# Optimization experiments

Hardware: AMD Instinct MI355X
Metric: run time of the kernel (lower is better)

The kernel has to match this reference:

```python
import jax, jax.numpy as jnp
import numpy as np

V, E, H, D = 10000, 256, 512, 768  # vocab, embed, hidden(=attn), encoder dims
B, T, N = 32, 128, 196


def setup_inputs() -> dict:
    key = jax.random.key(0)
    ks = jax.random.split(key, 16)
    s = 0.02
    inp = {
        "x": jax.random.randint(ks[0], (B, T), 0, V),
        "enc_mem": jax.random.normal(ks[1], (B, N, D), dtype=jnp.float32),
        "enc_mask": jnp.ones((B, N), dtype=jnp.int32),
        # parameters, stored (in, out) so y = x @ W
        "emb_table": jax.random.normal(ks[2], (V, E), dtype=jnp.float32) * s,
        "We": jax.random.normal(ks[3], (D, H), dtype=jnp.float32) * s,   # attn.W_e
        "Wh": jax.random.normal(ks[4], (H, H), dtype=jnp.float32) * s,   # attn.W_h
        "v": jax.random.normal(ks[5], (H,), dtype=jnp.float32) * s,      # attn.v
        "Wih": jax.random.normal(ks[6], (E + D, 4 * H), dtype=jnp.float32) * s,
        "Whh": jax.random.normal(ks[7], (H, 4 * H), dtype=jnp.float32) * s,
        "bih": jnp.zeros((4 * H,), dtype=jnp.float32),
        "bhh": jnp.zeros((4 * H,), dtype=jnp.float32),
        "fcW": jax.random.normal(ks[8], (H, V), dtype=jnp.float32) * s,
        "fcb": jnp.zeros((V,), dtype=jnp.float32),
        "W2h": jax.random.normal(ks[9], (D, H), dtype=jnp.float32) * s,  # enc_to_h
        "b2h": jnp.zeros((H,), dtype=jnp.float32),
        "W2c": jax.random.normal(ks[10], (D, H), dtype=jnp.float32) * s,  # enc_to_c
        "b2c": jnp.zeros((H,), dtype=jnp.float32),
    }
    return inp


def _decode(x, enc_mem, enc_mask, emb_table, We, Wh, v, Wih, Whh, bih, bhh,
            fcW, fcb, W2h, b2h, W2c, b2c):
    emb = emb_table[x]                       # (B,T,E); dropout=0 (eval)
    pooled = enc_mem.mean(axis=1)            # (B,D)
    h = jnp.tanh(pooled @ W2h + b2h)         # init_hidden
    c = jnp.tanh(pooled @ W2c + b2c)
    Ke = jnp.einsum('bnd,dh->bnh', enc_mem, We)  # precompute W_e(enc_mem)
    neg = jnp.float32(-1e9)
    mask0 = (enc_mask == 0)

    def step(carry, e_t):
        h, c = carry
        energy = jnp.tanh((h @ Wh)[:, None, :] + Ke)        # (B,N,H)
        scores = jnp.einsum('bnh,h->bn', energy, v)         # (B,N)
        scores = jnp.where(mask0, neg, scores)
        alpha = jax.nn.softmax(scores, axis=-1)
        context = jnp.einsum('bn,bnd->bd', alpha, enc_mem)  # (B,D)
        lstm_in = jnp.concatenate([e_t, context], axis=-1)  # (B,E+D)
        gates = lstm_in @ Wih + bih + h @ Whh + bhh         # (B,4H)
        i_g, f_g, g_g, o_g = jnp.split(gates, 4, axis=-1)   # torch order i,f,g,o
        c_new = jax.nn.sigmoid(f_g) * c + jax.nn.sigmoid(i_g) * jnp.tanh(g_g)
        h_new = jax.nn.sigmoid(o_g) * jnp.tanh(c_new)
        logit = h_new @ fcW + fcb                           # (B,V)
        return (h_new, c_new), logit

    (h, c), logits_t = jax.lax.scan(step, (h, c), jnp.swapaxes(emb, 0, 1))
    logits = jnp.swapaxes(logits_t, 0, 1)                   # (B,T,V)
    return logits, h, c


def reference(x, enc_mem, enc_mask, emb_table, We, Wh, v, Wih, Whh, bih, bhh,
              fcW, fcb, W2h, b2h, W2c, b2c):
    return _decode(x, enc_mem, enc_mask, emb_table, We, Wh, v, Wih, Whh,
                   bih, bhh, fcW, fcb, W2h, b2h, W2c, b2c)
```

## Files before the change

kernel.cpp:

```cpp
#include <hip/hip_runtime.h>

typedef unsigned short u16;
typedef __attribute__((ext_vector_type(8))) short short8;
typedef __attribute__((ext_vector_type(4))) float f32x4;
typedef __attribute__((ext_vector_type(4))) unsigned int u32x4;

#define B_  32
#define T_  128
#define N_  196
#define D_  768
#define E_  256
#define H_  512
#define V_  10000
#define G4H 2048
#define NBLK 256
#define BH  (B_ * H_)
#define BD  (B_ * D_)

#define O_ENCBF 0UL
#define O_WHT   9633792UL
#define O_WHHT  10158080UL
#define O_WIHDT 12255232UL
#define O_KE    15400960UL
#define O_GEMB  21823488UL
#define O_BSUM  38600704UL
#define O_CT    38608896UL
#define O_HIST  38674432UL
#define O_HX2   42868736UL
#define O_HWX   42934272UL
#define O_CTXA  42999808UL
#define O_DEN   43196416UL
#define O_BARS  43196672UL
#define O_REL   43198720UL

__device__ __forceinline__ float b2f(u16 u) {
  union { unsigned i; float f; } c; c.i = ((unsigned)u) << 16; return c.f;
}
__device__ __forceinline__ u16 f2b(float f) {
  unsigned u = __float_as_uint(f);
  unsigned r = (u + 0x7fffu + ((u >> 16) & 1u)) >> 16;
  return (u16)r;
}
__device__ __forceinline__ float fast_tanh(float x) {
  float e = __expf(2.f * x);
  return 1.f - 2.f * __builtin_amdgcn_rcpf(e + 1.f);
}
__device__ __forceinline__ float sigm(float x) {
  return __builtin_amdgcn_rcpf(1.f + __expf(-x));
}
__device__ __forceinline__ float wred_sum(float x) {
  #pragma unroll
  for (int o = 32; o; o >>= 1) x += __shfl_xor(x, o, 64);
  return x;
}

__device__ __forceinline__ float ld_bypass_f32(const float* p) {
  float v;
  asm volatile("global_load_dword %0, %1, off sc0 sc1\n\ts_waitcnt vmcnt(0)"
               : "=v"(v) : "v"(p) : "memory");
  return v;
}
__device__ __forceinline__ unsigned ld_bypass_u32(const unsigned* p) {
  unsigned v;
  asm volatile("global_load_dword %0, %1, off sc0 sc1\n\ts_waitcnt vmcnt(0)"
               : "=v"(v) : "v"(p) : "memory");
  return v;
}
__device__ __forceinline__ void ld2_bypass(const void* p0, const void* p1,
                                           u32x4& a, u32x4& b) {
  asm volatile(
    "global_load_dwordx4 %0, %2, off sc0 sc1\n\t"
    "global_load_dwordx4 %1, %3, off sc0 sc1\n\t"
    "s_waitcnt vmcnt(0)"
    : "=&v"(a), "=&v"(b) : "v"(p0), "v"(p1) : "memory");
}
__device__ __forceinline__ void ld6_1_bypass(
    const void* p0, const void* p1, const void* p2, const void* p3,
    const void* p4, const void* p5, const void* pd,
    u32x4& a, u32x4& b, u32x4& c, u32x4& d, u32x4& e, u32x4& f, float& dv) {
  asm volatile(
    "global_load_dwordx4 %0, %7, off sc0 sc1\n\t"
    "global_load_dwordx4 %1, %8, off sc0 sc1\n\t"
    "global_load_dwordx4 %2, %9, off sc0 sc1\n\t"
    "global_load_dwordx4 %3, %10, off sc0 sc1\n\t"
    "global_load_dwordx4 %4, %11, off sc0 sc1\n\t"
    "global_load_dwordx4 %5, %12, off sc0 sc1\n\t"
    "global_load_dword %6, %13, off sc0 sc1\n\t"
    "s_waitcnt vmcnt(0)"
    : "=&v"(a), "=&v"(b), "=&v"(c), "=&v"(d), "=&v"(e), "=&v"(f), "=&v"(dv)
    : "v"(p0), "v"(p1), "v"(p2), "v"(p3), "v"(p4), "v"(p5), "v"(pd)
    : "memory");
}
__device__ __forceinline__ void st_bypass_f32(float* p, float v) {
  asm volatile("global_store_dword %0, %1, off sc0 sc1" :: "v"(p), "v"(v) : "memory");
}
__device__ __forceinline__ void st_bypass_u32(unsigned* p, unsigned v) {
  asm volatile("global_store_dword %0, %1, off sc0 sc1" :: "v"(p), "v"(v) : "memory");
}
__device__ __forceinline__ void st_bypass_u16(u16* p, u16 v) {
  unsigned vv = v;
  asm volatile("global_store_short %0, %1, off sc0 sc1" :: "v"(p), "v"(vv) : "memory");
}

__device__ __forceinline__ unsigned bar_sum16(const unsigned* p) {
  unsigned a0,a1,a2,a3,a4,a5,a6,a7,a8,a9,a10,a11,a12,a13,a14,a15;
  asm volatile(
    "global_load_dword %0, %16, off sc0 sc1\n\t"
    "global_load_dword %1, %16, off offset:128 sc0 sc1\n\t"
    "global_load_dword %2, %16, off offset:256 sc0 sc1\n\t"
    "global_load_dword %3, %16, off offset:384 sc0 sc1\n\t"
    "global_load_dword %4, %16, off offset:512 sc0 sc1\n\t"
    "global_load_dword %5, %16, off offset:640 sc0 sc1\n\t"
    "global_load_dword %6, %16, off offset:768 sc0 sc1\n\t"
    "global_load_dword %7, %16, off offset:896 sc0 sc1\n\t"
    "global_load_dword %8, %16, off offset:1024 sc0 sc1\n\t"
    "global_load_dword %9, %16, off offset:1152 sc0 sc1\n\t"
    "global_load_dword %10, %16, off offset:1280 sc0 sc1\n\t"
    "global_load_dword %11, %16, off offset:1408 sc0 sc1\n\t"
    "global_load_dword %12, %16, off offset:1536 sc0 sc1\n\t"
    "global_load_dword %13, %16, off offset:1664 sc0 sc1\n\t"
    "global_load_dword %14, %16, off offset:1792 sc0 sc1\n\t"
    "global_load_dword %15, %16, off offset:1920 sc0 sc1\n\t"
    "s_waitcnt vmcnt(0)"
    : "=&v"(a0), "=&v"(a1), "=&v"(a2), "=&v"(a3), "=&v"(a4), "=&v"(a5),
      "=&v"(a6), "=&v"(a7), "=&v"(a8), "=&v"(a9), "=&v"(a10), "=&v"(a11),
      "=&v"(a12), "=&v"(a13), "=&v"(a14), "=&v"(a15)
    : "v"(p) : "memory");
  return ((a0+a1)+(a2+a3)) + ((a4+a5)+(a6+a7)) +
         ((a8+a9)+(a10+a11)) + ((a12+a13)+(a14+a15));
}

__device__ __forceinline__ void gridbar(unsigned* bars, unsigned* rel,
                                        int bid, unsigned target) {
  __syncthreads();
  if (bid == 0) {
    if (threadIdx.x == 0) {
      asm volatile("s_waitcnt vmcnt(0) lgkmcnt(0)" ::: "memory");
      __hip_atomic_fetch_add(bars, 1u, __ATOMIC_RELAXED, __HIP_MEMORY_SCOPE_AGENT);
      while (bar_sum16(bars) < target) __builtin_amdgcn_s_sleep(1);
    }
    __syncthreads();
    if (threadIdx.x < NBLK) st_bypass_u32(rel + (size_t)threadIdx.x * 32, target);
  } else {
    if (threadIdx.x == 0) {
      asm volatile("s_waitcnt vmcnt(0) lgkmcnt(0)" ::: "memory");
      __hip_atomic_fetch_add(bars + (size_t)(bid & 15) * 32, 1u,
                             __ATOMIC_RELAXED, __HIP_MEMORY_SCOPE_AGENT);
      while (ld_bypass_u32(rel + (size_t)bid * 32) < target)
        __builtin_amdgcn_s_sleep(2);
    }
    __syncthreads();
  }
}


__global__ void conv_bf(const float* __restrict__ in, u16* __restrict__ out, int n) {
  int i = blockIdx.x * blockDim.x + threadIdx.x;
  int st = gridDim.x * blockDim.x;
  for (; i < n; i += st) out[i] = f2b(in[i]);
}

__global__ void bsum_k(const float* __restrict__ a, const float* __restrict__ b,
                       float* __restrict__ o, int n) {
  int i = blockIdx.x * blockDim.x + threadIdx.x;
  if (i < n) o[i] = a[i] + b[i];
}

__global__ void transpose_bf(const float* __restrict__ in, u16* __restrict__ out, int R, int C) {
  __shared__ float tl[64][65];
  int tid = threadIdx.x;
  int tc0 = blockIdx.x * 64, tr0 = blockIdx.y * 64;
  int cc = tid & 63;
  for (int rr = tid >> 6; rr < 64; rr += 4) {
    int rg = tr0 + rr, cg = tc0 + cc;
    tl[rr][cc] = (rg < R && cg < C) ? in[(size_t)rg * C + cg] : 0.f;
  }
  __syncthreads();
  int rr = tid & 63;
  for (int c2 = tid >> 6; c2 < 64; c2 += 4) {
    int cg = tc0 + c2, rg = tr0 + rr;
    if (cg < C && rg < R) out[(size_t)cg * R + rg] = f2b(tl[rr][c2]);
  }
}

__global__ __launch_bounds__(512) void init_hc(
    const float* __restrict__ enc, const float* __restrict__ W2h,
    const float* __restrict__ b2h, const float* __restrict__ W2c,
    const float* __restrict__ b2c, u16* __restrict__ hx2, float* __restrict__ cT)
{
  __shared__ float pool[D_];
  int b = blockIdx.x, tid = threadIdx.x;
  for (int d = tid; d < D_; d += 512) {
    float s = 0.f;
    const float* ep = enc + (size_t)b * N_ * D_ + d;
    for (int n = 0; n < N_; ++n) s += ep[(size_t)n * D_];
    pool[d] = s * (1.f / 196.f);
  }
  __syncthreads();
  float a = b2h[tid], a2 = b2c[tid];
  #pragma unroll 4
  for (int d = 0; d < D_; ++d) {
    float pv = pool[d];
    a  += pv * W2h[d * H_ + tid];
    a2 += pv * W2c[d * H_ + tid];
  }
  hx2[b * H_ + tid] = f2b(fast_tanh(a));
  cT[b * H_ + tid] = fast_tanh(a2);
}

template<int AMODE, int OUTMODE, int BIAS>
__global__ __launch_bounds__(256) void gemm2(
    const void* __restrict__ Av, const float* __restrict__ Bf,
    const int* __restrict__ xidx, void* __restrict__ Cv,
    const float* __restrict__ bias, int M, int N, int K, int lda)
{
  __shared__ __align__(16) u16 Al[128][72];
  __shared__ __align__(16) u16 Bl[128][72];
  const int tid = threadIdx.x;
  const int tm0 = blockIdx.y * 128, tn0 = blockIdx.x * 128;
  const int wv = tid >> 6, lane = tid & 63;
  const int wr = wv >> 1, wc = wv & 1;
  f32x4 acc[4][4] = {};
  const int r = tid >> 1, cb = (tid & 1) * 32;
  const int bkr = tid >> 5;
  const int bnc = (tid & 31) * 4;
  for (int k0 = 0; k0 < K; k0 += 64) {
    int rm = tm0 + r; if (rm >= M) rm = M - 1;
    if (AMODE == 0) {
      const u16* gp = (const u16*)Av + (size_t)rm * lda + k0 + cb;
      #pragma unroll
      for (int u = 0; u < 4; ++u)
        *(short8*)&Al[r][cb + u * 8] = *(const short8*)(gp + u * 8);
    } else {
      const float* gp = (const float*)Av + (size_t)xidx[rm] * lda + k0 + cb;
      #pragma unroll
      for (int u = 0; u < 4; ++u) {
        f32x4 a0 = *(const f32x4*)(gp + u * 8);
        f32x4 a1 = *(const f32x4*)(gp + u * 8 + 4);
        Al[r][cb + u * 8 + 0] = f2b(a0[0]); Al[r][cb + u * 8 + 1] = f2b(a0[1]);
        Al[r][cb + u * 8 + 2] = f2b(a0[2]); Al[r][cb + u * 8 + 3] = f2b(a0[3]);
        Al[r][cb + u * 8 + 4] = f2b(a1[0]); Al[r][cb + u * 8 + 5] = f2b(a1[1]);
        Al[r][cb + u * 8 + 6] = f2b(a1[2]); Al[r][cb + u * 8 + 7] = f2b(a1[3]);
      }
    }
    {
      int ncc = tn0 + bnc; if (ncc > N - 4) ncc = N - 4;
      #pragma unroll
      for (int u = 0; u < 8; ++u) {
        int kr = bkr + u * 8;
        const float* bp = Bf + (size_t)(k0 + kr) * N + ncc;
        f32x4 bv = *(const f32x4*)bp;
        #pragma unroll
        for (int j = 0; j < 4; ++j) Bl[bnc + j][kr] = f2b(bv[j]);
      }
    }
    __syncthreads();
    #pragma unroll
    for (int kk = 0; kk < 64; kk += 32) {
      short8 af[4], bfv[4];
      #pragma unroll
      for (int i = 0; i < 4; ++i)
        af[i] = *(const short8*)&Al[wr * 64 + i * 16 + (lane & 15)][kk + (lane >> 4) * 8];
      #pragma unroll
      for (int j = 0; j < 4; ++j)
        bfv[j] = *(const short8*)&Bl[wc * 64 + j * 16 + (lane & 15)][kk + (lane >> 4) * 8];
      #pragma unroll
      for (int i = 0; i < 4; ++i)
        #pragma unroll
        for (int j = 0; j < 4; ++j)
          acc[i][j] = __builtin_amdgcn_mfma_f32_16x16x32_bf16(af[i], bfv[j], acc[i][j], 0, 0, 0);
    }
    __syncthreads();
  }
  #pragma unroll
  for (int i = 0; i < 4; ++i) {
    int row0 = tm0 + wr * 64 + i * 16 + (lane >> 4) * 4;
    #pragma unroll
    for (int j = 0; j < 4; ++j) {
      int col = tn0 + wc * 64 + j * 16 + (lane & 15);
      if (col < N) {
        float bs = BIAS ? bias[col] : 0.f;
        #pragma unroll
        for (int rr2 = 0; rr2 < 4; ++rr2) {
          int row = row0 + rr2;
          if (row < M) {
            float val = acc[i][j][rr2] + bs;
            if (OUTMODE == 0) ((float*)Cv)[(size_t)row * N + col] = val;
            else if (OUTMODE == 1) ((u16*)Cv)[(size_t)row * N + col] = f2b(val);
            else {
              int tt = row & 127, bb = row >> 7;
              ((u16*)Cv)[((size_t)tt * G4H + col) * 32 + bb] = f2b(val);
            }
          }
        }
      }
    }
  }
}

__global__ __launch_bounds__(512, 1) void recur9(
    const u16* __restrict__ enc_bf, const int* __restrict__ mask,
    const u16* __restrict__ Ke, const u16* __restrict__ WhT,
    const float* __restrict__ vvec, const u16* __restrict__ WhhT,
    const u16* __restrict__ WihDT, const u16* __restrict__ g_emb,
    const float* __restrict__ cT0,
    u16* hx2, float* hwx, float* ctxAcc, float* denom,
    u16* h_hist, float* out_h, float* out_c, unsigned* bars, unsigned* rel)
{
  __shared__ u32x4 hst16[64 * 16];
  __shared__ union {
    struct { float part1[8][64]; } p1;
    struct { float hw8[512]; float e[32]; } p2;
    struct { u32x4 ctx16[96 * 16]; f32x4 part3[8][69]; } p3;
  } su;
  __shared__ float gpre[16][16];
  __shared__ float cfl[4][16];
  __shared__ float maskf[32];

  const int bid = blockIdx.x, tid = threadIdx.x;
  const int lane = tid & 63, wvx = tid >> 6;
  const int b = bid >> 3, s8 = bid & 7;
  const int n0 = s8 * 25;
  const int nmax = min(25, N_ - n0);
  const int bh = bid >> 7, hb4 = bid & 127;
  const int b_base = bh * 16, hx4 = hb4 * 4;
  const int n16 = lane & 15, kh = lane >> 4;
  const int gcol = (n16 >> 2) * H_ + hx4 + (n16 & 3);
  const int hb16 = tid & 15, hc4 = (tid >> 4) & 3, hks = tid >> 6;
  const int hwc = hb4 * 4 + hc4;
  const int bl = tid & 15, kc0 = tid >> 4;
  const int ro = tid & 15, co = tid >> 4;

  float vreg[8];
  #pragma unroll
  for (int j = 0; j < 8; ++j) vreg[j] = vvec[lane * 8 + j];
  if (tid < nmax) maskf[tid] = (mask[b * N_ + n0 + tid] == 0) ? 0.f : 1.f;
  if (tid < 64) cfl[tid >> 4][tid & 15] =
      cT0[(b_base + (tid & 15)) * H_ + hx4 + (tid >> 4)];

  short8 wf[5];
  #pragma unroll
  for (int i = 0; i < 5; ++i) {
    int ks = wvx * 5 + i;
    if (ks < 16) wf[i] = *(const short8*)(WhhT + (size_t)gcol * H_ + ks * 32 + kh * 8);
    else         wf[i] = *(const short8*)(WihDT + (size_t)gcol * D_ + (ks - 16) * 32 + kh * 8);
  }
  short8 wh8[8];
  #pragma unroll
  for (int i = 0; i < 8; ++i)
    wh8[i] = *(const short8*)(WhT + (size_t)hwc * H_ + hks * 64 + i * 8);
  short8 kvp[4];
  #pragma unroll
  for (int i = 0; i < 4; ++i) {
    int nn = wvx + i * 8; if (nn >= nmax) nn = nmax - 1;
    kvp[i] = *(const short8*)(Ke + ((size_t)(b * N_ + n0 + nn)) * H_ + lane * 8);
  }
  __syncthreads();

  unsigned tgt = 0;
  for (int t = 0; t < T_; ++t) {
    const int rb = t & 1, wb = rb ^ 1;
    const int cbuf = t & 1, nbuf = cbuf ^ 1;
    {
      const u16* hp = hx2 + (size_t)rb * BH + (b_base + bl) * H_;
      u32x4 v0, v1;
      ld2_bypass(hp + kc0 * 8, hp + (kc0 + 32) * 8, v0, v1);
      hst16[(kc0     ) * 16 + bl] = v0;
      hst16[(kc0 + 32) * 16 + bl] = v1;
    }
    __syncthreads();
    {
      float acc = 0.f;
      #pragma unroll
      for (int i = 0; i < 8; ++i) {
        short8 hb8 = *(const short8*)&hst16[(hks * 8 + i) * 16 + hb16];
        #pragma unroll
        for (int j = 0; j < 8; ++j)
          acc += b2f((u16)wh8[i][j]) * b2f((u16)hb8[j]);
      }
      su.p1.part1[hks][hc4 * 16 + hb16] = acc;
    }
    __syncthreads();
    if (tid < 64) {
      float s = 0.f;
      #pragma unroll
      for (int w = 0; w < 8; ++w) s += su.p1.part1[w][tid];
      st_bypass_f32(hwx + (size_t)(b_base + (tid & 15)) * H_ + hb4 * 4 + (tid >> 4), s);
    }
    tgt += NBLK;
    f32x4 gacc = {0.f, 0.f, 0.f, 0.f};
    float ge_pf = 0.f;
    __syncthreads();
    if (tid == 0) {
      asm volatile("s_waitcnt vmcnt(0) lgkmcnt(0)" ::: "memory");
      __hip_atomic_fetch_add(bars + (size_t)(bid & 15) * 32, 1u,
                             __ATOMIC_RELAXED, __HIP_MEMORY_SCOPE_AGENT);
    }
    if (bid == 0) {
      if (tid == 0) { while (bar_sum16(bars) < tgt) __builtin_amdgcn_s_sleep(1); }
      __syncthreads();
      if (tid < NBLK) st_bypass_u32(rel + (size_t)tid * 32, tgt);
      #pragma unroll
      for (int i = 0; i < 5; ++i) {
        int ks = wvx * 5 + i;
        if (ks < 16)
          gacc = __builtin_amdgcn_mfma_f32_16x16x32_bf16(
              *(const short8*)&hst16[(ks * 4 + kh) * 16 + n16], wf[i], gacc, 0, 0, 0);
      }
      if (tid < 256) {
        int gco = (co >> 2) * H_ + hx4 + (co & 3);
        ge_pf = b2f(g_emb[((size_t)t * G4H + gco) * 32 + (b_base + ro)]);
      }
    } else {
      #pragma unroll
      for (int i = 0; i < 5; ++i) {
        int ks = wvx * 5 + i;
        if (ks < 16)
          gacc = __builtin_amdgcn_mfma_f32_16x16x32_bf16(
              *(const short8*)&hst16[(ks * 4 + kh) * 16 + n16], wf[i], gacc, 0, 0, 0);
      }
      if (tid < 256) {
        int gco = (co >> 2) * H_ + hx4 + (co & 3);
        ge_pf = b2f(g_emb[((size_t)t * G4H + gco) * 32 + (b_base + ro)]);
      }
      __syncthreads();
      if (tid == 0) {
        while (ld_bypass_u32(rel + (size_t)bid * 32) < tgt)
          __builtin_amdgcn_s_sleep(2);
      }
      __syncthreads();
    }

    su.p2.hw8[(tid & 7) * 64 + (tid >> 3)] = ld_bypass_f32(hwx + b * H_ + tid);
    if (tid >= 25 && tid < 32) su.p2.e[tid] = 0.f;
    __syncthreads();
    #pragma unroll
    for (int i = 0; i < 4; ++i) {
      int nn = wvx + i * 8;
      if (nn < nmax) {
        float p = 0.f;
        #pragma unroll
        for (int j = 0; j < 8; ++j)
          p += vreg[j] * fast_tanh(su.p2.hw8[j * 64 + lane] + b2f((u16)kvp[i][j]));
        p = wred_sum(p);
        if (lane == 0) su.p2.e[nn] = maskf[nn] * __expf(p);
      }
    }
    __syncthreads();
    if (wvx == 0) {
      float sp = (lane < 25) ? su.p2.e[lane] : 0.f;
      sp = wred_sum(sp);
      if (lane == 0) atomicAdd(denom + cbuf * 32 + b, sp);
    }
    if (tid < 384) {
      float a0 = 0.f, a1 = 0.f;
      const u16* ep0 = enc_bf + ((size_t)(b * N_ + n0)) * D_ + 2 * tid;
      #pragma unroll
      for (int nn = 0; nn < 25; ++nn) {
        int nn_c = (nn < nmax) ? nn : 0;
        float ev = su.p2.e[nn];
        unsigned w = *(const unsigned*)(ep0 + (size_t)nn_c * D_);
        a0 += ev * b2f((u16)(w & 0xffffu));
        a1 += ev * b2f((u16)(w >> 16));
      }
      float* cp = ctxAcc + (size_t)cbuf * BD + b * D_ + 2 * tid;
      atomicAdd(cp, a0);
      atomicAdd(cp + 1, a1);
    }
    tgt += NBLK; gridbar(bars, rel, bid, tgt);

    {
      const float* cp = ctxAcc + (size_t)cbuf * BD + (size_t)(b_base + bl) * D_;
      u32x4 ca[3][2]; float dv;
      ld6_1_bypass(cp + (kc0     ) * 8, cp + (kc0     ) * 8 + 4,
                   cp + (kc0 + 32) * 8, cp + (kc0 + 32) * 8 + 4,
                   cp + (kc0 + 64) * 8, cp + (kc0 + 64) * 8 + 4,
                   denom + cbuf * 32 + (b_base + bl),
                   ca[0][0], ca[0][1], ca[1][0], ca[1][1],
                   ca[2][0], ca[2][1], dv);
      float rdv = 1.f / dv;
      #pragma unroll
      for (int r2 = 0; r2 < 3; ++r2) {
        int kc = kc0 + r2 * 32;
        u32x4 pk;
        #pragma unroll
        for (int hh = 0; hh < 2; ++hh) {
          float x0 = __uint_as_float(ca[r2][hh][0]) * rdv;
          float x1 = __uint_as_float(ca[r2][hh][1]) * rdv;
          float x2 = __uint_as_float(ca[r2][hh][2]) * rdv;
          float x3 = __uint_as_float(ca[r2][hh][3]) * rdv;
          pk[hh * 2]     = (unsigned)f2b(x0) | ((unsigned)f2b(x1) << 16);
          pk[hh * 2 + 1] = (unsigned)f2b(x2) | ((unsigned)f2b(x3) << 16);
        }
        su.p3.ctx16[kc * 16 + bl] = pk;
      }
    }
    __syncthreads();
    #pragma unroll
    for (int i = 0; i < 5; ++i) {
      int ks = wvx * 5 + i;
      if (ks >= 16)
        gacc = __builtin_amdgcn_mfma_f32_16x16x32_bf16(
            *(const short8*)&su.p3.ctx16[((ks - 16) * 4 + kh) * 16 + n16], wf[i],
            gacc, 0, 0, 0);
    }
    *(f32x4*)&su.p3.part3[wvx][lane] = gacc;
    __syncthreads();
    if (tid < 256) {
      int lp = ((ro >> 2) << 4) | co;
      float v = su.p3.part3[0][lp][ro & 3] + su.p3.part3[1][lp][ro & 3]
              + su.p3.part3[2][lp][ro & 3] + su.p3.part3[3][lp][ro & 3]
              + su.p3.part3[4][lp][ro & 3] + su.p3.part3[5][lp][ro & 3]
              + su.p3.part3[6][lp][ro & 3] + su.p3.part3[7][lp][ro & 3];
      gpre[co][ro] = v + ge_pf;
    }
    __syncthreads();
    if (tid < 64) {
      int row = tid & 15, j = tid >> 4;
      float gI = gpre[j][row], gF = gpre[4 + j][row];
      float gG = gpre[8 + j][row], gO = gpre[12 + j][row];
      float co2 = cfl[j][row];
      float cn = sigm(gF) * co2 + sigm(gI) * fast_tanh(gG);
      float hn = sigm(gO) * fast_tanh(cn);
      cfl[j][row] = cn;
      int bgl = b_base + row, hidx = hx4 + j;
      st_bypass_u16(hx2 + (size_t)wb * BH + bgl * H_ + hidx, f2b(hn));
      h_hist[((size_t)(bgl * T_ + t)) * H_ + hidx] = f2b(hn);
      if (t == T_ - 1) {
        out_h[bgl * H_ + hidx] = hn;
        out_c[bgl * H_ + hidx] = cn;
      }
    }
    tgt += NBLK;
    __syncthreads();
    if (tid == 0) {
      asm volatile("s_waitcnt vmcnt(0) lgkmcnt(0)" ::: "memory");
      __hip_atomic_fetch_add(bars + (size_t)(bid & 15) * 32, 1u,
                             __ATOMIC_RELAXED, __HIP_MEMORY_SCOPE_AGENT);
    }
    if (bid == 0) {
      if (tid == 0) { while (bar_sum16(bars) < tgt) __builtin_amdgcn_s_sleep(1); }
      __syncthreads();
      if (tid < NBLK) st_bypass_u32(rel + (size_t)tid * 32, tgt);
      if (tid < 96) st_bypass_f32(ctxAcc + (size_t)nbuf * BD + bid * 96 + tid, 0.f);
      if (tid < 32) st_bypass_f32(denom + nbuf * 32 + tid, 0.f);
    } else {
      if (tid < 96) st_bypass_f32(ctxAcc + (size_t)nbuf * BD + bid * 96 + tid, 0.f);
      __syncthreads();
      if (tid == 0) {
        while (ld_bypass_u32(rel + (size_t)bid * 32) < tgt)
          __builtin_amdgcn_s_sleep(2);
      }
      __syncthreads();
    }
  }
}

extern "C" void kernel_launch(void* const* d_in, const int* in_sizes, int n_in,
                              void* d_out, int out_size, void* d_ws, size_t ws_size,
                              hipStream_t stream) {
  const int*   x    = (const int*)d_in[0];
  const float* enc  = (const float*)d_in[1];
  const int*   mask = (const int*)d_in[2];
  const float* emb  = (const float*)d_in[3];
  const float* We   = (const float*)d_in[4];
  const float* Wh   = (const float*)d_in[5];
  const float* v    = (const float*)d_in[6];
  const float* Wih  = (const float*)d_in[7];
  const float* Whh  = (const float*)d_in[8];
  const float* bih  = (const float*)d_in[9];
  const float* bhh  = (const float*)d_in[10];
  const float* fcW  = (const float*)d_in[11];
  const float* fcb  = (const float*)d_in[12];
  const float* W2h  = (const float*)d_in[13];
  const float* b2h  = (const float*)d_in[14];
  const float* W2c  = (const float*)d_in[15];
  const float* b2c  = (const float*)d_in[16];
  float* out = (float*)d_out;

  char* ws = (char*)d_ws;
  u16* enc_bf = (u16*)(ws + O_ENCBF);
  u16* WhT    = (u16*)(ws + O_WHT);
  u16* WhhT   = (u16*)(ws + O_WHHT);
  u16* WihDT  = (u16*)(ws + O_WIHDT);
  u16* Ke     = (u16*)(ws + O_KE);
  u16* g_emb  = (u16*)(ws + O_GEMB);
  float* bsum = (float*)(ws + O_BSUM);
  float* cT   = (float*)(ws + O_CT);
  u16* h_hist = (u16*)(ws + O_HIST);
  u16* hx2    = (u16*)(ws + O_HX2);
  float* hwx  = (float*)(ws + O_HWX);
  float* ctxAcc = (float*)(ws + O_CTXA);
  float* denom  = (float*)(ws + O_DEN);
  unsigned* bars = (unsigned*)(ws + O_BARS);
  unsigned* rel  = (unsigned*)(ws + O_REL);
  float* out_h = out + (size_t)B_ * T_ * V_;
  float* out_c = out_h + B_ * H_;

  hipMemsetAsync(bars, 0, 2048, stream);
  hipMemsetAsync(rel, 0, 32768, stream);
  hipMemsetAsync(ctxAcc, 0, 196608, stream);
  hipMemsetAsync(denom, 0, 256, stream);
  conv_bf<<<1024, 256, 0, stream>>>(enc, enc_bf, B_ * N_ * D_);
  transpose_bf<<<dim3(8, 8), 256, 0, stream>>>(Wh, WhT, H_, H_);
  transpose_bf<<<dim3(32, 8), 256, 0, stream>>>(Whh, WhhT, H_, G4H);
  transpose_bf<<<dim3(32, 12), 256, 0, stream>>>(Wih + (size_t)E_ * G4H, WihDT, D_, G4H);
  bsum_k<<<8, 256, 0, stream>>>(bih, bhh, bsum, G4H);
  init_hc<<<32, 512, 0, stream>>>(enc, W2h, b2h, W2c, b2c, hx2, cT);
  gemm2<0, 1, 0><<<dim3(4, 49), 256, 0, stream>>>(enc_bf, We, nullptr, (void*)Ke,
                                                  nullptr, B_ * N_, H_, D_, D_);
  gemm2<1, 3, 1><<<dim3(16, 32), 256, 0, stream>>>(emb, Wih, x, (void*)g_emb,
                                                   bsum, B_ * T_, G4H, E_, E_);
  recur9<<<NBLK, 512, 0, stream>>>(enc_bf, mask, Ke, WhT, v, WhhT, WihDT, g_emb,
                                   cT, hx2, hwx, ctxAcc, denom,
                                   h_hist, out_h, out_c, bars, rel);
  gemm2<0, 0, 1><<<dim3(79, 32), 256, 0, stream>>>(h_hist, fcW, nullptr, (void*)out,
                                                   fcb, B_ * T_, V_, H_, H_);
}
```

Before: 2.512 ms.

## Replace master-polled grid barrier with hierarchical last-arriver release

The grid barrier no longer has block 0 repeatedly summing 16 counters before releasing everyone. Each block atomically increments its group counter, and the last arriver in a group bumps a summary counter. Whichever block arrives last overall writes the release flags for all 256 blocks. This removes the master's polling latency from the critical path of each of the three barriers per timestep, at the cost of serial release stores from a single thread and an extra atomic on the summary counter.

Result: slower. 3.357 ms (+33.6%).

```diff
diff --git a/kernel.cpp b/kernel.cpp
--- a/kernel.cpp
+++ b/kernel.cpp
@@ -32,6 +32,7 @@
 #define O_DEN   43196416UL
 #define O_BARS  43196672UL
 #define O_REL   43198720UL
+#define O_SUM   43231488UL
 
 __device__ __forceinline__ float b2f(u16 u) {
   union { unsigned i; float f; } c; c.i = ((unsigned)u) << 16; return c.f;
@@ -102,55 +103,30 @@
   asm volatile("global_store_short %0, %1, off sc0 sc1" :: "v"(p), "v"(vv) : "memory");
 }
 
-__device__ __forceinline__ unsigned bar_sum16(const unsigned* p) {
-  unsigned a0,a1,a2,a3,a4,a5,a6,a7,a8,a9,a10,a11,a12,a13,a14,a15;
-  asm volatile(
-    "global_load_dword %0, %16, off sc0 sc1\n\t"
-    "global_load_dword %1, %16, off offset:128 sc0 sc1\n\t"
-    "global_load_dword %2, %16, off offset:256 sc0 sc1\n\t"
-    "global_load_dword %3, %16, off offset:384 sc0 sc1\n\t"
-    "global_load_dword %4, %16, off offset:512 sc0 sc1\n\t"
-    "global_load_dword %5, %16, off offset:640 sc0 sc1\n\t"
-    "global_load_dword %6, %16, off offset:768 sc0 sc1\n\t"
-    "global_load_dword %7, %16, off offset:896 sc0 sc1\n\t"
-    "global_load_dword %8, %16, off offset:1024 sc0 sc1\n\t"
-    "global_load_dword %9, %16, off offset:1152 sc0 sc1\n\t"
-    "global_load_dword %10, %16, off offset:1280 sc0 sc1\n\t"
-    "global_load_dword %11, %16, off offset:1408 sc0 sc1\n\t"
-    "global_load_dword %12, %16, off offset:1536 sc0 sc1\n\t"
-    "global_load_dword %13, %16, off offset:1664 sc0 sc1\n\t"
-    "global_load_dword %14, %16, off offset:1792 sc0 sc1\n\t"
-    "global_load_dword %15, %16, off offset:1920 sc0 sc1\n\t"
-    "s_waitcnt vmcnt(0)"
-    : "=&v"(a0), "=&v"(a1), "=&v"(a2), "=&v"(a3), "=&v"(a4), "=&v"(a5),
-      "=&v"(a6), "=&v"(a7), "=&v"(a8), "=&v"(a9), "=&v"(a10), "=&v"(a11),
-      "=&v"(a12), "=&v"(a13), "=&v"(a14), "=&v"(a15)
-    : "v"(p) : "memory");
-  return ((a0+a1)+(a2+a3)) + ((a4+a5)+(a6+a7)) +
-         ((a8+a9)+(a10+a11)) + ((a12+a13)+(a14+a15));
-}
-
-__device__ __forceinline__ void gridbar(unsigned* bars, unsigned* rel,
-                                        int bid, unsigned target) {
+__device__ __forceinline__ void bar_arrive(unsigned* bars, unsigned* summary,
+                                           unsigned* rel, int bid, unsigned bk) {
   __syncthreads();
-  if (bid == 0) {
-    if (threadIdx.x == 0) {
-      asm volatile("s_waitcnt vmcnt(0) lgkmcnt(0)" ::: "memory");
-      __hip_atomic_fetch_add(bars, 1u, __ATOMIC_RELAXED, __HIP_MEMORY_SCOPE_AGENT);
-      while (bar_sum16(bars) < target) __builtin_amdgcn_s_sleep(1);
-    }
-    __syncthreads();
-    if (threadIdx.x < NBLK) st_bypass_u32(rel + (size_t)threadIdx.x * 32, target);
-  } else {
-    if (threadIdx.x == 0) {
-      asm volatile("s_waitcnt vmcnt(0) lgkmcnt(0)" ::: "memory");
-      __hip_atomic_fetch_add(bars + (size_t)(bid & 15) * 32, 1u,
-                             __ATOMIC_RELAXED, __HIP_MEMORY_SCOPE_AGENT);
-      while (ld_bypass_u32(rel + (size_t)bid * 32) < target)
-        __builtin_amdgcn_s_sleep(2);
-    }
-    __syncthreads();
-  }
+  if (threadIdx.x == 0) {
+    asm volatile("s_waitcnt vmcnt(0) lgkmcnt(0)" ::: "memory");
+    unsigned r = __hip_atomic_fetch_add(bars + (size_t)(bid & 15) * 32, 1u,
+                                        __ATOMIC_RELAXED, __HIP_MEMORY_SCOPE_AGENT);
+    if (r + 1u == 16u * bk) {
+      unsigned s = __hip_atomic_fetch_add(summary, 1u, __ATOMIC_RELAXED,
+                                          __HIP_MEMORY_SCOPE_AGENT);
+      if (s + 1u == 16u * bk) {
+        #pragma unroll 8
+        for (int i = 0; i < NBLK; ++i)
+          st_bypass_u32(rel + (size_t)i * 32, bk);
+      }
+    }
+  }
+}
+__device__ __forceinline__ void bar_wait(unsigned* rel, int bid, unsigned bk) {
+  if (threadIdx.x == 0) {
+    while (ld_bypass_u32(rel + (size_t)bid * 32) < bk)
+      __builtin_amdgcn_s_sleep(1);
+  }
+  __syncthreads();
 }
 
 
@@ -298,14 +274,15 @@
   }
 }
 
-__global__ __launch_bounds__(512, 1) void recur9(
+__global__ __launch_bounds__(512, 1) void recur10(
     const u16* __restrict__ enc_bf, const int* __restrict__ mask,
     const u16* __restrict__ Ke, const u16* __restrict__ WhT,
     const float* __restrict__ vvec, const u16* __restrict__ WhhT,
     const u16* __restrict__ WihDT, const u16* __restrict__ g_emb,
     const float* __restrict__ cT0,
     u16* hx2, float* hwx, float* ctxAcc, float* denom,
-    u16* h_hist, float* out_h, float* out_c, unsigned* bars, unsigned* rel)
+    u16* h_hist, float* out_h, float* out_c,
+    unsigned* bars, unsigned* summary, unsigned* rel)
 {
   __shared__ u32x4 hst16[64 * 16];
   __shared__ union {
@@ -357,7 +334,7 @@
   }
   __syncthreads();
 
-  unsigned tgt = 0;
+  unsigned bk = 0;
   for (int t = 0; t < T_; ++t) {
     const int rb = t & 1, wb = rb ^ 1;
     const int cbuf = t & 1, nbuf = cbuf ^ 1;
@@ -387,49 +364,22 @@
       for (int w = 0; w < 8; ++w) s += su.p1.part1[w][tid];
       st_bypass_f32(hwx + (size_t)(b_base + (tid & 15)) * H_ + hb4 * 4 + (tid >> 4), s);
     }
-    tgt += NBLK;
+    ++bk;
+    bar_arrive(bars, summary, rel, bid, bk);
     f32x4 gacc = {0.f, 0.f, 0.f, 0.f};
     float ge_pf = 0.f;
-    __syncthreads();
-    if (tid == 0) {
-      asm volatile("s_waitcnt vmcnt(0) lgkmcnt(0)" ::: "memory");
-      __hip_atomic_fetch_add(bars + (size_t)(bid & 15) * 32, 1u,
-                             __ATOMIC_RELAXED, __HIP_MEMORY_SCOPE_AGENT);
-    }
-    if (bid == 0) {
-      if (tid == 0) { while (bar_sum16(bars) < tgt) __builtin_amdgcn_s_sleep(1); }
-      __syncthreads();
-      if (tid < NBLK) st_bypass_u32(rel + (size_t)tid * 32, tgt);
-      #pragma unroll
-      for (int i = 0; i < 5; ++i) {
-        int ks = wvx * 5 + i;
-        if (ks < 16)
-          gacc = __builtin_amdgcn_mfma_f32_16x16x32_bf16(
-              *(const short8*)&hst16[(ks * 4 + kh) * 16 + n16], wf[i], gacc, 0, 0, 0);
-      }
-      if (tid < 256) {
-        int gco = (co >> 2) * H_ + hx4 + (co & 3);
-        ge_pf = b2f(g_emb[((size_t)t * G4H + gco) * 32 + (b_base + ro)]);
-      }
-    } else {
-      #pragma unroll
-      for (int i = 0; i < 5; ++i) {
-        int ks = wvx * 5 + i;
-        if (ks < 16)
-          gacc = __builtin_amdgcn_mfma_f32_16x16x32_bf16(
-              *(const short8*)&hst16[(ks * 4 + kh) * 16 + n16], wf[i], gacc, 0, 0, 0);
-      }
-      if (tid < 256) {
-        int gco = (co >> 2) * H_ + hx4 + (co & 3);
-        ge_pf = b2f(g_emb[((size_t)t * G4H + gco) * 32 + (b_base + ro)]);
-      }
-      __syncthreads();
-      if (tid == 0) {
-        while (ld_bypass_u32(rel + (size_t)bid * 32) < tgt)
-          __builtin_amdgcn_s_sleep(2);
-      }
-      __syncthreads();
-    }
+    #pragma unroll
+    for (int i = 0; i < 5; ++i) {
+      int ks = wvx * 5 + i;
+      if (ks < 16)
+        gacc = __builtin_amdgcn_mfma_f32_16x16x32_bf16(
+            *(const short8*)&hst16[(ks * 4 + kh) * 16 + n16], wf[i], gacc, 0, 0, 0);
+    }
+    if (tid < 256) {
+      int gco = (co >> 2) * H_ + hx4 + (co & 3);
+      ge_pf = b2f(g_emb[((size_t)t * G4H + gco) * 32 + (b_base + ro)]);
+    }
+    bar_wait(rel, bid, bk);
 
     su.p2.hw8[(tid & 7) * 64 + (tid >> 3)] = ld_bypass_f32(hwx + b * H_ + tid);
     if (tid >= 25 && tid < 32) su.p2.e[tid] = 0.f;
@@ -467,7 +417,9 @@
       atomicAdd(cp, a0);
       atomicAdd(cp + 1, a1);
     }
-    tgt += NBLK; gridbar(bars, rel, bid, tgt);
+    ++bk;
+    bar_arrive(bars, summary, rel, bid, bk);
+    bar_wait(rel, bid, bk);
 
     {
       const float* cp = ctxAcc + (size_t)cbuf * BD + (size_t)(b_base + bl) * D_;
@@ -531,28 +483,11 @@
         out_c[bgl * H_ + hidx] = cn;
       }
     }
-    tgt += NBLK;
-    __syncthreads();
-    if (tid == 0) {
-      asm volatile("s_waitcnt vmcnt(0) lgkmcnt(0)" ::: "memory");
-      __hip_atomic_fetch_add(bars + (size_t)(bid & 15) * 32, 1u,
-                             __ATOMIC_RELAXED, __HIP_MEMORY_SCOPE_AGENT);
-    }
-    if (bid == 0) {
-      if (tid == 0) { while (bar_sum16(bars) < tgt) __builtin_amdgcn_s_sleep(1); }
-      __syncthreads();
-      if (tid < NBLK) st_bypass_u32(rel + (size_t)tid * 32, tgt);
-      if (tid < 96) st_bypass_f32(ctxAcc + (size_t)nbuf * BD + bid * 96 + tid, 0.f);
-      if (tid < 32) st_bypass_f32(denom + nbuf * 32 + tid, 0.f);
-    } else {
-      if (tid < 96) st_bypass_f32(ctxAcc + (size_t)nbuf * BD + bid * 96 + tid, 0.f);
-      __syncthreads();
-      if (tid == 0) {
-        while (ld_bypass_u32(rel + (size_t)bid * 32) < tgt)
-          __builtin_amdgcn_s_sleep(2);
-      }
-      __syncthreads();
-    }
+    ++bk;
+    bar_arrive(bars, summary, rel, bid, bk);
+    if (tid < 96) st_bypass_f32(ctxAcc + (size_t)nbuf * BD + bid * 96 + tid, 0.f);
+    if (bid == 0 && tid < 32) st_bypass_f32(denom + nbuf * 32 + tid, 0.f);
+    bar_wait(rel, bid, bk);
   }
 }
 
@@ -594,11 +529,13 @@
   float* denom  = (float*)(ws + O_DEN);
   unsigned* bars = (unsigned*)(ws + O_BARS);
   unsigned* rel  = (unsigned*)(ws + O_REL);
+  unsigned* summary = (unsigned*)(ws + O_SUM);
   float* out_h = out + (size_t)B_ * T_ * V_;
   float* out_c = out_h + B_ * H_;
 
   hipMemsetAsync(bars, 0, 2048, stream);
   hipMemsetAsync(rel, 0, 32768, stream);
+  hipMemsetAsync(summary, 0, 128, stream);
   hipMemsetAsync(ctxAcc, 0, 196608, stream);
   hipMemsetAsync(denom, 0, 256, stream);
   conv_bf<<<1024, 256, 0, stream>>>(enc, enc_bf, B_ * N_ * D_);
@@ -611,9 +548,9 @@
                                                   nullptr, B_ * N_, H_, D_, D_);
   gemm2<1, 3, 1><<<dim3(16, 32), 256, 0, stream>>>(emb, Wih, x, (void*)g_emb,
                                                    bsum, B_ * T_, G4H, E_, E_);
-  recur9<<<NBLK, 512, 0, stream>>>(enc_bf, mask, Ke, WhT, v, WhhT, WihDT, g_emb,
-                                   cT, hx2, hwx, ctxAcc, denom,
-                                   h_hist, out_h, out_c, bars, rel);
+  recur10<<<NBLK, 512, 0, stream>>>(enc_bf, mask, Ke, WhT, v, WhhT, WihDT, g_emb,
+                                    cT, hx2, hwx, ctxAcc, denom,
+                                    h_hist, out_h, out_c, bars, summary, rel);
   gemm2<0, 0, 1><<<dim3(79, 32), 256, 0, stream>>>(h_hist, fcW, nullptr, (void*)out,
                                                    fcb, B_ * T_, V_, H_, H_);
 }
```
